# Kernel optimization log

Measured on AMD Instinct MI355X. Metric: run time of the kernel, lower is better.

## Reference

```python
import jax, jax.numpy as jnp
import numpy as np
from jax import lax

B, P, N, D, L, H = 16, 8192, 1024, 384, 12, 6
HD = D // H
K_NEI = 5          # HomogeneityLoss k
KL_RATIO = 1.0


def setup_inputs() -> dict:
    key = jax.random.key(0)
    ks = jax.random.split(key, 10)
    s = lambda i, shape, sc=0.02: (jax.random.normal(ks[i], shape, jnp.float32) * sc)
    return dict(
        pts=jax.random.normal(ks[0], (B, P, 3), jnp.float32),
        grid=jax.random.normal(ks[1], (B, N, 3), jnp.float32),
        embed_w=s(2, (3, D), 0.1),
        proj_w=s(3, (D, 3), 0.1),
        ln1_w=jnp.ones((L, D)), ln1_b=jnp.zeros((L, D)),
        qkv_w=s(4, (L, D, 3 * D)), qkv_b=jnp.zeros((L, 3 * D)),
        attn_w=s(5, (L, D, D)), attn_b=jnp.zeros((L, D)),
        ln2_w=jnp.ones((L, D)), ln2_b=jnp.zeros((L, D)),
        mlp_w1=s(6, (L, D, 4 * D)), mlp_b1=jnp.zeros((L, 4 * D)),
        mlp_w2=s(7, (L, 4 * D, D)), mlp_b2=jnp.zeros((L, D)),
    )


def _ln(x, w, b):
    m = jnp.mean(x, -1, keepdims=True)
    v = jnp.var(x, -1, keepdims=True)
    return (x - m) * lax.rsqrt(v + 1e-5) * w + b


def _transformer(x, params):
    def layer(x, p):
        l1w, l1b, qw, qb, aw, ab, l2w, l2b, m1w, m1b, m2w, m2b = p
        h = _ln(x, l1w, l1b)
        qkv = h @ qw + qb                                   # [B,N,3D]
        q, k, v = jnp.split(qkv, 3, axis=-1)
        rs = lambda t: t.reshape(B, N, H, HD).transpose(0, 2, 1, 3)  # [B,H,N,HD]
        q, k, v = rs(q), rs(k), rs(v)
        att = jax.nn.softmax(jnp.einsum('bhnd,bhmd->bhnm', q, k) / np.sqrt(HD), axis=-1)
        o = jnp.einsum('bhnm,bhmd->bhnd', att, v).transpose(0, 2, 1, 3).reshape(B, N, D)
        x = x + (o @ aw + ab)
        h = _ln(x, l2w, l2b)
        x = x + (jax.nn.gelu(h @ m1w + m1b) @ m2w + m2b)
        return x, None
    x, _ = lax.scan(layer, x, params)
    return x


def _fps(points):  # points: [P,3] -> N int32 indices (farthest point sampling)
    def body(carry, _):
        dists, last = carry
        d = jnp.sum((points - points[last]) ** 2, axis=-1)
        dists = jnp.minimum(dists, d)
        return (dists, jnp.argmax(dists).astype(jnp.int32)), last
    init = (jnp.full((points.shape[0],), 1e10, points.dtype), jnp.int32(0))
    (_, _), idxs = lax.scan(body, init, None, length=N)
    return idxs


def reference(pts, grid, embed_w, proj_w, ln1_w, ln1_b, qkv_w, qkv_b,
              attn_w, attn_b, ln2_w, ln2_b, mlp_w1, mlp_b1, mlp_w2, mlp_b2):
    params = (ln1_w, ln1_b, qkv_w, qkv_b, attn_w, attn_b,
              ln2_w, ln2_b, mlp_w1, mlp_b1, mlp_w2, mlp_b2)
    x = grid @ embed_w                                      # [B,N,D]
    x = _transformer(x, params)
    pred = x @ proj_w                                       # [B,N,3]

    # FPS centers from the raw point cloud
    idxs = jax.vmap(_fps)(pts)                              # [B,N]
    centers = jnp.take_along_axis(pts, idxs[..., None], axis=1)  # [B,N,3]

    # Chamfer L1 (symmetric mean of nearest-neighbor L2 norms)
    d = jnp.linalg.norm(pred[:, :, None, :] - centers[:, None, :, :], axis=-1)  # [B,N,N]
    rec = 0.5 * (d.min(axis=2).mean(axis=1) + d.min(axis=1).mean(axis=1))       # [B]

    # Homogeneity: mean dist of K_NEI nearest neighbors -> softmax -> KL(q||p)
    dd = jnp.linalg.norm(pred[:, :, None, :] - pred[:, None, :, :], axis=-1)    # [B,N,N]
    neg_vals, _ = lax.top_k(-dd, K_NEI + 1)                 # smallest K+1 dists
    mean_d = (-neg_vals[..., 1:]).mean(axis=-1)             # drop self -> [B,N]
    logp = jax.nn.log_softmax(mean_d, axis=-1)
    q = 1.0 / N
    kl = jnp.sum(q * (jnp.log(q) - logp), axis=-1)          # [B]

    return rec.mean(), KL_RATIO * kl.mean()
```

## Files before the change

kernel.cpp:

```cpp
#include <hip/hip_runtime.h>
#include <math.h>

#define B_   16
#define P_   8192
#define N_   1024
#define D_   384
#define L_   12
#define H_   6
#define HD_  64
#define M_   (B_*N_)
#define DQKV_ (3*D_)
#define DH_   (4*D_)

typedef unsigned short ushort_t;
typedef unsigned long long u64_t;
typedef __attribute__((ext_vector_type(8))) short short8;
typedef __attribute__((ext_vector_type(4))) float floatx4;

__device__ __forceinline__ ushort_t f2bf(float f) {
    unsigned u = __float_as_uint(f);
    unsigned rounding = 0x7fffu + ((u >> 16) & 1u);
    return (ushort_t)((u + rounding) >> 16);
}
__device__ __forceinline__ float bf2f(ushort_t u) {
    return __uint_as_float(((unsigned)u) << 16);
}

__global__ __launch_bounds__(D_) void embed_kernel(const float* __restrict__ g,
                                                   const float* __restrict__ ew,
                                                   float* __restrict__ X) {
    int m = blockIdx.x;
    int d = threadIdx.x;
    float g0 = g[m*3+0], g1 = g[m*3+1], g2 = g[m*3+2];
    X[(size_t)m*D_ + d] = g0*ew[0*D_+d] + g1*ew[1*D_+d] + g2*ew[2*D_+d];
}

__global__ __launch_bounds__(256) void transcast_kernel(const float* __restrict__ W,
                                                        ushort_t* __restrict__ Wt,
                                                        int K, int Nc) {
    __shared__ float t[32][33];
    const float* Wl = W + (size_t)blockIdx.z*K*Nc;
    ushort_t* Wtl = Wt + (size_t)blockIdx.z*K*Nc;
    int n0 = blockIdx.x*32, k0 = blockIdx.y*32;
    int tx = threadIdx.x & 31, ty = threadIdx.x >> 5;
#pragma unroll
    for (int j = 0; j < 32; j += 8)
        t[ty+j][tx] = Wl[(size_t)(k0+ty+j)*Nc + n0+tx];
    __syncthreads();
#pragma unroll
    for (int j = 0; j < 32; j += 8)
        Wtl[(size_t)(n0+ty+j)*K + k0+tx] = f2bf(t[tx][ty+j]);
}

__global__ __launch_bounds__(256) void ln_kernel(const float* __restrict__ Xin,
                                                 const float* __restrict__ w,
                                                 const float* __restrict__ bvec,
                                                 ushort_t* __restrict__ out) {
    int wid = threadIdx.x >> 6, lane = threadIdx.x & 63;
    int row = blockIdx.x*4 + wid;
    const float* xr = Xin + (size_t)row*D_;
    float v[6];
#pragma unroll
    for (int i = 0; i < 6; i++) v[i] = xr[lane + i*64];
    float s = 0.f;
#pragma unroll
    for (int i = 0; i < 6; i++) s += v[i];
#pragma unroll
    for (int off = 32; off; off >>= 1) s += __shfl_xor(s, off, 64);
    float mean = s * (1.0f/(float)D_);
    float vs = 0.f;
#pragma unroll
    for (int i = 0; i < 6; i++) { float d = v[i]-mean; vs += d*d; }
#pragma unroll
    for (int off = 32; off; off >>= 1) vs += __shfl_xor(vs, off, 64);
    float var = vs * (1.0f/(float)D_);
    float rstd = 1.0f / sqrtf(var + 1e-5f);
    ushort_t* orow = out + (size_t)row*D_;
#pragma unroll
    for (int i = 0; i < 6; i++) {
        int e = lane + i*64;
        orow[e] = f2bf((v[i]-mean)*rstd*w[e] + bvec[e]);
    }
}

__device__ __forceinline__ float gelu_f(float x) {
    const float c = 0.7978845608028654f;
    float x3 = x*x*x;
    return 0.5f*x*(1.0f + tanhf(c*(x + 0.044715f*x3)));
}

template<int EPI>
__global__ __launch_bounds__(256) void mfma_gemm(const ushort_t* __restrict__ A,
                                                 const ushort_t* __restrict__ Wt,
                                                 const float* __restrict__ bias,
                                                 void* __restrict__ Cout,
                                                 ushort_t* __restrict__ VT,
                                                 int K, int Nc) {
    __shared__ __attribute__((aligned(16))) ushort_t smem[2*128*32];
    ushort_t* smA = smem;
    ushort_t* smB = smem + 128*32;
    int tid = threadIdx.x;
    int lane = tid & 63, w = tid >> 6;
    int wm = w >> 1, wn = w & 1;
    int L = lane & 15, G = lane >> 4;
    int rowBase = blockIdx.y * 128, colBase = blockIdx.x * 128;

    floatx4 acc[4][4];
#pragma unroll
    for (int i = 0; i < 4; i++)
#pragma unroll
        for (int j = 0; j < 4; j++) acc[i][j] = (floatx4){0.f,0.f,0.f,0.f};

    int sr = tid >> 2;
    int kc = tid & 3;
    const ushort_t* Ag = A  + (size_t)(rowBase + sr)*K + kc*8;
    const ushort_t* Bg = Wt + (size_t)(colBase + sr)*K + kc*8;
    size_t step64 = (size_t)64*K;

    short8 ra0, ra1, rb0, rb1;
    ra0 = *(const short8*)(Ag);
    ra1 = *(const short8*)(Ag + step64);
    rb0 = *(const short8*)(Bg);
    rb1 = *(const short8*)(Bg + step64);

    for (int k0 = 0; k0 < K; k0 += 32) {
        __syncthreads();
        *(short8*)(smA + sr*32 + kc*8)        = ra0;
        *(short8*)(smA + (64+sr)*32 + kc*8)   = ra1;
        *(short8*)(smB + sr*32 + kc*8)        = rb0;
        *(short8*)(smB + (64+sr)*32 + kc*8)   = rb1;
        __syncthreads();
        if (k0 + 32 < K) {
            ra0 = *(const short8*)(Ag + k0 + 32);
            ra1 = *(const short8*)(Ag + step64 + k0 + 32);
            rb0 = *(const short8*)(Bg + k0 + 32);
            rb1 = *(const short8*)(Bg + step64 + k0 + 32);
        }
        short8 af[4], bfr[4];
#pragma unroll
        for (int t = 0; t < 4; t++) {
            af[t]  = *(const short8*)(smA + (wm*64 + t*16 + L)*32 + G*8);
            bfr[t] = *(const short8*)(smB + (wn*64 + t*16 + L)*32 + G*8);
        }
#pragma unroll
        for (int mt = 0; mt < 4; mt++)
#pragma unroll
            for (int nt = 0; nt < 4; nt++)
                acc[mt][nt] = __builtin_amdgcn_mfma_f32_16x16x32_bf16(
                    af[mt], bfr[nt], acc[mt][nt], 0, 0, 0);
        __syncthreads();
    }

    __syncthreads();

    if (EPI == 3 && colBase >= 2*D_) {
        int cBase = colBase + wn*64 + L;
        int rBase = rowBase + wm*64 + G*4;
#pragma unroll
        for (int nt = 0; nt < 4; nt++) {
            int col = cBase + nt*16;
            float bv = bias[col];
            int hh = (col - 2*D_) >> 6, d = (col - 2*D_) & 63;
#pragma unroll
            for (int mt = 0; mt < 4; mt++) {
#pragma unroll
                for (int r = 0; r < 4; r++) {
                    int row = rBase + mt*16 + r;
                    int b = row >> 10, n = row & 1023;
                    VT[(((size_t)b*H_ + hh)*64 + d)*N_ + n] = f2bf(acc[mt][nt][r] + bv);
                }
            }
        }
    } else if (EPI == 1) {
        float* fs = (float*)smem + w*1024;
        int orow = lane >> 2, c4 = lane & 3;
#pragma unroll
        for (int mt = 0; mt < 4; mt++) {
#pragma unroll
            for (int nt = 0; nt < 4; nt++) {
                float bv = bias[colBase + wn*64 + nt*16 + L];
#pragma unroll
                for (int r = 0; r < 4; r++)
                    fs[(G*4+r)*64 + nt*16 + L] = acc[mt][nt][r] + bv;
            }
            float* og = (float*)Cout + (size_t)(rowBase + wm*64 + mt*16 + orow)*Nc
                        + colBase + wn*64;
#pragma unroll
            for (int kk = 0; kk < 4; kk++) {
                float4 sv = *(float4*)(fs + orow*64 + kk*16 + c4*4);
                float4 gv = *(float4*)(og + kk*16 + c4*4);
                gv.x += sv.x; gv.y += sv.y; gv.z += sv.z; gv.w += sv.w;
                *(float4*)(og + kk*16 + c4*4) = gv;
            }
        }
    } else {
        ushort_t* us = smem + w*1152;
        int orow = lane >> 2, oc = lane & 3;
#pragma unroll
        for (int mt = 0; mt < 4; mt++) {
#pragma unroll
            for (int nt = 0; nt < 4; nt++) {
                float bv = bias[colBase + wn*64 + nt*16 + L];
#pragma unroll
                for (int r = 0; r < 4; r++) {
                    float v = acc[mt][nt][r] + bv;
                    if (EPI == 2) v = gelu_f(v);
                    us[(G*4+r)*72 + nt*16 + L] = f2bf(v);
                }
            }
            short8 o0 = *(short8*)(us + orow*72 + oc*8);
            short8 o1 = *(short8*)(us + orow*72 + 32 + oc*8);
            ushort_t* og = (ushort_t*)Cout + (size_t)(rowBase + wm*64 + mt*16 + orow)*Nc
                           + colBase + wn*64;
            *(short8*)(og + oc*8) = o0;
            *(short8*)(og + 32 + oc*8) = o1;
        }
    }
}

#define LPAD 72
__global__ __launch_bounds__(256) void fattn_kernel(const ushort_t* __restrict__ QKV,
                                                    const ushort_t* __restrict__ VT,
                                                    ushort_t* __restrict__ O) {
    __shared__ __attribute__((aligned(16))) ushort_t Ks[64*LPAD];
    __shared__ __attribute__((aligned(16))) ushort_t Vs[64*LPAD];
    __shared__ __attribute__((aligned(16))) ushort_t Pw[4*16*LPAD];
    int b = blockIdx.z, h = blockIdx.y;
    int qBase = blockIdx.x * 64;
    int tid = threadIdx.x;
    int lane = tid & 63, w = tid >> 6;
    int L = lane & 15, G = lane >> 4;

    short8 qf[2];
    {
        const ushort_t* qp = QKV + ((size_t)(b*N_ + qBase + w*16 + L))*DQKV_ + h*HD_ + G*8;
        qf[0] = *(const short8*)(qp);
        qf[1] = *(const short8*)(qp + 32);
    }

    floatx4 oacc[4];
#pragma unroll
    for (int nt = 0; nt < 4; nt++) oacc[nt] = (floatx4){0.f,0.f,0.f,0.f};
    float mrow[4], lrow[4];
#pragma unroll
    for (int r = 0; r < 4; r++) { mrow[r] = -3.0e38f; lrow[r] = 0.f; }

    ushort_t* pw = Pw + w*16*LPAD;
    const ushort_t* Kbase = QKV + (size_t)b*N_*DQKV_ + D_ + h*HD_;
    const ushort_t* Vbase = VT + ((size_t)b*H_ + h)*64*N_;

    int srow = tid >> 3;
    int dc   = tid & 7;
    const ushort_t* Kg0 = Kbase + (size_t)srow*DQKV_ + dc*8;
    const ushort_t* Kg1 = Kbase + (size_t)(srow+32)*DQKV_ + dc*8;
    const ushort_t* Vg0 = Vbase + (size_t)srow*N_ + dc*8;
    const ushort_t* Vg1 = Vbase + (size_t)(srow+32)*N_ + dc*8;

    short8 rk0, rk1, rv0, rv1;
    rk0 = *(const short8*)(Kg0);
    rk1 = *(const short8*)(Kg1);
    rv0 = *(const short8*)(Vg0);
    rv1 = *(const short8*)(Vg1);

    for (int kt = 0; kt < N_/64; kt++) {
        __syncthreads();
        *(short8*)(Ks + srow*LPAD + dc*8)       = rk0;
        *(short8*)(Ks + (srow+32)*LPAD + dc*8)  = rk1;
        *(short8*)(Vs + srow*LPAD + dc*8)       = rv0;
        *(short8*)(Vs + (srow+32)*LPAD + dc*8)  = rv1;
        __syncthreads();
        if (kt + 1 < N_/64) {
            rk0 = *(const short8*)(Kg0 + (size_t)(kt+1)*64*DQKV_);
            rk1 = *(const short8*)(Kg1 + (size_t)(kt+1)*64*DQKV_);
            rv0 = *(const short8*)(Vg0 + (kt+1)*64);
            rv1 = *(const short8*)(Vg1 + (kt+1)*64);
        }

        floatx4 sc[4];
#pragma unroll
        for (int ct = 0; ct < 4; ct++) sc[ct] = (floatx4){0.f,0.f,0.f,0.f};
#pragma unroll
        for (int ks = 0; ks < 2; ks++)
#pragma unroll
            for (int ct = 0; ct < 4; ct++) {
                short8 bf = *(const short8*)(Ks + (ct*16 + L)*LPAD + ks*32 + G*8);
                sc[ct] = __builtin_amdgcn_mfma_f32_16x16x32_bf16(qf[ks], bf, sc[ct], 0, 0, 0);
            }

        float rmax[4], rsum[4];
#pragma unroll
        for (int r = 0; r < 4; r++) {
#pragma unroll
            for (int ct = 0; ct < 4; ct++) sc[ct][r] *= 0.125f;
            rmax[r] = fmaxf(fmaxf(sc[0][r], sc[1][r]), fmaxf(sc[2][r], sc[3][r]));
        }
#pragma unroll
        for (int off = 1; off < 16; off <<= 1)
#pragma unroll
            for (int r = 0; r < 4; r++) rmax[r] = fmaxf(rmax[r], __shfl_xor(rmax[r], off, 64));
        float corr[4];
#pragma unroll
        for (int r = 0; r < 4; r++) {
            float mn = fmaxf(mrow[r], rmax[r]);
            corr[r] = __expf(mrow[r] - mn);
            mrow[r] = mn;
            rsum[r] = 0.f;
#pragma unroll
            for (int ct = 0; ct < 4; ct++) {
                float p = __expf(sc[ct][r] - mn);
                sc[ct][r] = p;
                rsum[r] += p;
            }
        }
#pragma unroll
        for (int off = 1; off < 16; off <<= 1)
#pragma unroll
            for (int r = 0; r < 4; r++) rsum[r] += __shfl_xor(rsum[r], off, 64);
#pragma unroll
        for (int r = 0; r < 4; r++) lrow[r] = lrow[r]*corr[r] + rsum[r];

#pragma unroll
        for (int ct = 0; ct < 4; ct++)
#pragma unroll
            for (int r = 0; r < 4; r++)
                pw[(G*4 + r)*LPAD + ct*16 + L] = f2bf(sc[ct][r]);
#pragma unroll
        for (int nt = 0; nt < 4; nt++)
#pragma unroll
            for (int r = 0; r < 4; r++) oacc[nt][r] *= corr[r];

#pragma unroll
        for (int ks = 0; ks < 2; ks++) {
            short8 pf = *(const short8*)(pw + L*LPAD + ks*32 + G*8);
#pragma unroll
            for (int nt = 0; nt < 4; nt++) {
                short8 vf = *(const short8*)(Vs + (nt*16 + L)*LPAD + ks*32 + G*8);
                oacc[nt] = __builtin_amdgcn_mfma_f32_16x16x32_bf16(pf, vf, oacc[nt], 0, 0, 0);
            }
        }
    }

    float inv[4];
#pragma unroll
    for (int r = 0; r < 4; r++) inv[r] = 1.0f / lrow[r];
#pragma unroll
    for (int nt = 0; nt < 4; nt++)
#pragma unroll
        for (int r = 0; r < 4; r++)
            pw[(G*4 + r)*LPAD + nt*16 + L] = f2bf(oacc[nt][r]*inv[r]);
    int orow = lane >> 2, oc = lane & 3;
    short8 o0 = *(short8*)(pw + orow*LPAD + oc*8);
    short8 o1 = *(short8*)(pw + orow*LPAD + 32 + oc*8);
    ushort_t* og = O + (size_t)(b*N_ + qBase + w*16 + orow)*D_ + h*HD_;
    *(short8*)(og + oc*8) = o0;
    *(short8*)(og + 32 + oc*8) = o1;
}

__global__ __launch_bounds__(256) void proj_kernel(const float* __restrict__ X,
                                                   const float* __restrict__ pw,
                                                   float* __restrict__ pred) {
    int wid = threadIdx.x >> 6, lane = threadIdx.x & 63;
    int m = blockIdx.x*4 + wid;
    const float* xr = X + (size_t)m*D_;
    float a0 = 0.f, a1 = 0.f, a2 = 0.f;
#pragma unroll
    for (int i = 0; i < 6; i++) {
        int k = lane + i*64;
        float xv = xr[k];
        a0 += xv*pw[k*3+0]; a1 += xv*pw[k*3+1]; a2 += xv*pw[k*3+2];
    }
#pragma unroll
    for (int off = 32; off; off >>= 1) {
        a0 += __shfl_xor(a0, off, 64);
        a1 += __shfl_xor(a1, off, 64);
        a2 += __shfl_xor(a2, off, 64);
    }
    if (lane == 0) {
        pred[m*3+0] = a0; pred[m*3+1] = a1; pred[m*3+2] = a2;
    }
}

__global__ __launch_bounds__(512) void fps_kernel(const float* __restrict__ pts,
                                                  float* __restrict__ centers) {
    __shared__ float Lx[P_], Ly[P_], Lz[P_];
    __shared__ u64_t slot[2][8];
    int b = blockIdx.x, t = threadIdx.x;
    const float* pb = pts + (size_t)b*P_*3;
    float px[16], py[16], pz[16], dist[16];
#pragma unroll
    for (int j = 0; j < 16; j++) {
        int p = j*512 + t;
        px[j] = pb[p*3+0]; py[j] = pb[p*3+1]; pz[j] = pb[p*3+2];
        Lx[p] = px[j]; Ly[p] = py[j]; Lz[p] = pz[j];
        dist[j] = 1e10f;
    }
    int wid = t >> 6, lane = t & 63;
    int winner = 0;
    __syncthreads();
    for (int it = 0; it < N_; it++) {
        float lx = Lx[winner], ly = Ly[winner], lz = Lz[winner];
        if (t == 0) {
            float* c = centers + ((size_t)b*N_ + it)*3;
            c[0] = lx; c[1] = ly; c[2] = lz;
        }
        float bd = -1.0f; int bj = 0;
#pragma unroll
        for (int j = 0; j < 16; j++) {
            float dx = __fsub_rn(px[j], lx);
            float dy = __fsub_rn(py[j], ly);
            float dz = __fsub_rn(pz[j], lz);
            float d = __fadd_rn(__fadd_rn(__fmul_rn(dx,dx), __fmul_rn(dy,dy)), __fmul_rn(dz,dz));
            d = fminf(dist[j], d);
            dist[j] = d;
            bool gt = d > bd;
            bd = gt ? d : bd;
            bj = gt ? j : bj;
        }
        u64_t best = ((u64_t)__float_as_uint(bd) << 32)
                   | (unsigned)(~(unsigned)(bj*512 + t));
#pragma unroll
        for (int off = 32; off; off >>= 1) {
            u64_t o = __shfl_xor(best, off, 64);
            best = (o > best) ? o : best;
        }
        int par = it & 1;
        if (lane == 0) slot[par][wid] = best;
        __syncthreads();
        u64_t v = slot[par][lane & 7];
#pragma unroll
        for (int off = 1; off < 8; off <<= 1) {
            u64_t o = __shfl_xor(v, off, 64);
            v = (o > v) ? o : v;
        }
        winner = (int)(~(unsigned)(v & 0xFFFFFFFFull));
    }
}

__global__ __launch_bounds__(256) void nnmin_kernel(const float* __restrict__ Asrc,
                                                    const float* __restrict__ Bsrc,
                                                    float* __restrict__ outmin) {
    int b = blockIdx.y;
    int i = blockIdx.x*256 + threadIdx.x;
    __shared__ float tile[256][3];
    const float* ar = Asrc + ((size_t)b*N_ + i)*3;
    float ax = ar[0], ay = ar[1], az = ar[2];
    float best = 3.0e38f;
    for (int j0 = 0; j0 < N_; j0 += 256) {
        __syncthreads();
        const float* br = Bsrc + ((size_t)b*N_ + j0 + threadIdx.x)*3;
        tile[threadIdx.x][0] = br[0]; tile[threadIdx.x][1] = br[1]; tile[threadIdx.x][2] = br[2];
        __syncthreads();
        for (int j = 0; j < 256; j++) {
            float dx = ax - tile[j][0], dy = ay - tile[j][1], dz = az - tile[j][2];
            float d = dx*dx + dy*dy + dz*dz;
            best = fminf(best, d);
        }
    }
    outmin[(size_t)b*N_ + i] = sqrtf(best);
}

__global__ __launch_bounds__(256) void knn_kernel(const float* __restrict__ Pp,
                                                  float* __restrict__ mean_d) {
    int b = blockIdx.y;
    int i = blockIdx.x*256 + threadIdx.x;
    __shared__ float tile[256][3];
    const float* ar = Pp + ((size_t)b*N_ + i)*3;
    float ax = ar[0], ay = ar[1], az = ar[2];
    float s[6];
#pragma unroll
    for (int q = 0; q < 6; q++) s[q] = 3.0e38f;
    for (int j0 = 0; j0 < N_; j0 += 256) {
        __syncthreads();
        const float* br = Pp + ((size_t)b*N_ + j0 + threadIdx.x)*3;
        tile[threadIdx.x][0] = br[0]; tile[threadIdx.x][1] = br[1]; tile[threadIdx.x][2] = br[2];
        __syncthreads();
        for (int j = 0; j < 256; j++) {
            float dx = ax - tile[j][0], dy = ay - tile[j][1], dz = az - tile[j][2];
            float d = dx*dx + dy*dy + dz*dz;
            if (d < s[5]) {
                s[5] = d;
#pragma unroll
                for (int q = 5; q > 0; q--)
                    if (s[q] < s[q-1]) { float tmp = s[q]; s[q] = s[q-1]; s[q-1] = tmp; }
            }
        }
    }
    float msum = sqrtf(s[1]) + sqrtf(s[2]) + sqrtf(s[3]) + sqrtf(s[4]) + sqrtf(s[5]);
    mean_d[(size_t)b*N_ + i] = msum * 0.2f;
}

__global__ __launch_bounds__(256) void kl_kernel(const float* __restrict__ md,
                                                 float* __restrict__ klb) {
    int b = blockIdx.x, t = threadIdx.x;
    const float* row = md + (size_t)b*N_;
    float v[4];
#pragma unroll
    for (int i = 0; i < 4; i++) v[i] = row[t + i*256];
    float mx = fmaxf(fmaxf(v[0], v[1]), fmaxf(v[2], v[3]));
#pragma unroll
    for (int off = 32; off; off >>= 1) mx = fmaxf(mx, __shfl_xor(mx, off, 64));
    __shared__ float redm[4], rse[4], rsx[4];
    int wid = t >> 6, lane = t & 63;
    if (lane == 0) redm[wid] = mx;
    __syncthreads();
    mx = fmaxf(fmaxf(redm[0], redm[1]), fmaxf(redm[2], redm[3]));
    float se = 0.f, sx = 0.f;
#pragma unroll
    for (int i = 0; i < 4; i++) { se += expf(v[i]-mx); sx += v[i]; }
#pragma unroll
    for (int off = 32; off; off >>= 1) { se += __shfl_xor(se, off, 64); sx += __shfl_xor(sx, off, 64); }
    if (lane == 0) { rse[wid] = se; rsx[wid] = sx; }
    __syncthreads();
    if (t == 0) {
        float SE = rse[0]+rse[1]+rse[2]+rse[3];
        float SX = rsx[0]+rsx[1]+rsx[2]+rsx[3];
        klb[b] = mx + logf(SE) - SX*(1.0f/(float)N_) - logf((float)N_);
    }
}

__global__ __launch_bounds__(256) void final_kernel(const float* __restrict__ rma,
                                                    const float* __restrict__ rmb,
                                                    const float* __restrict__ klb,
                                                    float* __restrict__ out) {
    int t = threadIdx.x;
    float s = 0.f;
    for (int i = t; i < B_*N_; i += 256) s += rma[i] + rmb[i];
#pragma unroll
    for (int off = 32; off; off >>= 1) s += __shfl_xor(s, off, 64);
    __shared__ float red[4];
    int wid = t >> 6, lane = t & 63;
    if (lane == 0) red[wid] = s;
    __syncthreads();
    if (t == 0) {
        float S = red[0]+red[1]+red[2]+red[3];
        out[0] = 0.5f*S/(float)(B_*N_);
        float K = 0.f;
        for (int b = 0; b < B_; b++) K += klb[b];
        out[1] = K/(float)B_;
    }
}

extern "C" void kernel_launch(void* const* d_in, const int* in_sizes, int n_in,
                              void* d_out, int out_size, void* d_ws, size_t ws_size,
                              hipStream_t stream) {
    (void)in_sizes; (void)n_in; (void)out_size; (void)ws_size;
    const float* pts     = (const float*)d_in[0];
    const float* grid    = (const float*)d_in[1];
    const float* embed_w = (const float*)d_in[2];
    const float* proj_w  = (const float*)d_in[3];
    const float* ln1_w   = (const float*)d_in[4];
    const float* ln1_b   = (const float*)d_in[5];
    const float* qkv_w   = (const float*)d_in[6];
    const float* qkv_b   = (const float*)d_in[7];
    const float* attn_w  = (const float*)d_in[8];
    const float* attn_b  = (const float*)d_in[9];
    const float* ln2_w   = (const float*)d_in[10];
    const float* ln2_b   = (const float*)d_in[11];
    const float* mlp_w1  = (const float*)d_in[12];
    const float* mlp_b1  = (const float*)d_in[13];
    const float* mlp_w2  = (const float*)d_in[14];
    const float* mlp_b2  = (const float*)d_in[15];
    float* out = (float*)d_out;

    float*    X     = (float*)d_ws;
    ushort_t* Hb16  = (ushort_t*)(X + (size_t)M_*D_);
    ushort_t* BIG16 = Hb16 + (size_t)M_*D_;
    ushort_t* VT    = BIG16 + (size_t)M_*DH_;
    ushort_t* WQ    = VT  + (size_t)B_*H_*HD_*N_;
    ushort_t* WA    = WQ  + (size_t)L_*DQKV_*D_;
    ushort_t* WM1   = WA  + (size_t)L_*D_*D_;
    ushort_t* WM2   = WM1 + (size_t)L_*DH_*D_;
    float*    PRED  = (float*)(WM2 + (size_t)L_*D_*DH_);
    float*    CENT  = PRED + (size_t)M_*3;
    float*    RMA   = CENT + (size_t)B_*N_*3;
    float*    RMB   = RMA  + (size_t)B_*N_;
    float*    MEAND = RMB  + (size_t)B_*N_;
    float*    KLB   = MEAND + (size_t)B_*N_;

    transcast_kernel<<<dim3(DQKV_/32, D_/32,  L_), 256, 0, stream>>>(qkv_w,  WQ,  D_,  DQKV_);
    transcast_kernel<<<dim3(D_/32,    D_/32,  L_), 256, 0, stream>>>(attn_w, WA,  D_,  D_);
    transcast_kernel<<<dim3(DH_/32,   D_/32,  L_), 256, 0, stream>>>(mlp_w1, WM1, D_,  DH_);
    transcast_kernel<<<dim3(D_/32,    DH_/32, L_), 256, 0, stream>>>(mlp_w2, WM2, DH_, D_);

    fps_kernel<<<B_, 512, 0, stream>>>(pts, CENT);

    embed_kernel<<<M_, D_, 0, stream>>>(grid, embed_w, X);

    for (int l = 0; l < L_; l++) {
        ln_kernel<<<M_/4, 256, 0, stream>>>(X, ln1_w + l*D_, ln1_b + l*D_, Hb16);
        mfma_gemm<3><<<dim3(DQKV_/128, M_/128), 256, 0, stream>>>(
            Hb16, WQ + (size_t)l*DQKV_*D_, qkv_b + l*DQKV_, BIG16, VT, D_, DQKV_);
        fattn_kernel<<<dim3(N_/64, H_, B_), 256, 0, stream>>>(BIG16, VT, Hb16);
        mfma_gemm<1><<<dim3(D_/128, M_/128), 256, 0, stream>>>(
            Hb16, WA + (size_t)l*D_*D_, attn_b + l*D_, X, nullptr, D_, D_);
        ln_kernel<<<M_/4, 256, 0, stream>>>(X, ln2_w + l*D_, ln2_b + l*D_, Hb16);
        mfma_gemm<2><<<dim3(DH_/128, M_/128), 256, 0, stream>>>(
            Hb16, WM1 + (size_t)l*DH_*D_, mlp_b1 + l*DH_, BIG16, nullptr, D_, DH_);
        mfma_gemm<1><<<dim3(D_/128, M_/128), 256, 0, stream>>>(
            BIG16, WM2 + (size_t)l*D_*DH_, mlp_b2 + l*D_, X, nullptr, DH_, D_);
    }

    proj_kernel<<<M_/4, 256, 0, stream>>>(X, proj_w, PRED);

    nnmin_kernel<<<dim3(N_/256, B_), 256, 0, stream>>>(PRED, CENT, RMA);
    nnmin_kernel<<<dim3(N_/256, B_), 256, 0, stream>>>(CENT, PRED, RMB);
    knn_kernel<<<dim3(N_/256, B_), 256, 0, stream>>>(PRED, MEAND);
    kl_kernel<<<B_, 256, 0, stream>>>(MEAND, KLB);
    final_kernel<<<1, 256, 0, stream>>>(RMA, RMB, KLB, out);
}
```

Baseline: 4.619 ms.

## Split FPS into chunks piggybacked on transformer GEMM and attention launches

Removes the standalone serial FPS kernel and runs it in 29-iteration chunks inside extra blocks appended to the QKV GEMM, attention and MLP1 GEMM grids. Per-batch distance state and the current winner persist in global memory between chunks. The goal is to hide the long single-block-per-batch FPS latency behind the transformer work. In exchange, each chunk reloads point coordinates from global memory every iteration instead of holding them in LDS or registers. The extra blocks, placed at the end of the grid, may also lengthen the tail of each kernel they join.

```diff
diff --git a/kernel.cpp b/kernel.cpp
--- a/kernel.cpp
+++ b/kernel.cpp
@@ -11,6 +11,7 @@
 #define M_   (B_*N_)
 #define DQKV_ (3*D_)
 #define DH_   (4*D_)
+#define FPS_IT 29
 
 typedef unsigned short ushort_t;
 typedef unsigned long long u64_t;
@@ -24,6 +25,71 @@
 }
 __device__ __forceinline__ float bf2f(ushort_t u) {
     return __uint_as_float(((unsigned)u) << 16);
+}
+
+__device__ __forceinline__ void fps_chunk(const float* __restrict__ pts,
+                                          float* __restrict__ FDIST,
+                                          int* __restrict__ FWIN,
+                                          float* __restrict__ CENT,
+                                          int b, int start, u64_t* slot) {
+    int t = threadIdx.x;
+    int wid = t >> 6, lane = t & 63;
+    const float* pb = pts + (size_t)b*P_*3;
+    float* fd = FDIST + (size_t)b*P_;
+    float dist[32];
+    int winner;
+    if (start == 0) {
+#pragma unroll
+        for (int j = 0; j < 32; j++) dist[j] = 1e10f;
+        winner = 0;
+    } else {
+#pragma unroll
+        for (int j = 0; j < 32; j++) dist[j] = fd[j*256 + t];
+        winner = FWIN[b];
+    }
+    int end = start + FPS_IT; if (end > N_) end = N_;
+    for (int it = start; it < end; it++) {
+        const float* wc = pb + winner*3;
+        float lx = wc[0], ly = wc[1], lz = wc[2];
+        if (t == 0) {
+            float* c = CENT + ((size_t)b*N_ + it)*3;
+            c[0] = lx; c[1] = ly; c[2] = lz;
+        }
+        float bd = -1.0f; int bj = 0;
+#pragma unroll
+        for (int j = 0; j < 32; j++) {
+            int p = j*256 + t;
+            float dx = __fsub_rn(pb[p*3+0], lx);
+            float dy = __fsub_rn(pb[p*3+1], ly);
+            float dz = __fsub_rn(pb[p*3+2], lz);
+            float d = __fadd_rn(__fadd_rn(__fmul_rn(dx,dx), __fmul_rn(dy,dy)), __fmul_rn(dz,dz));
+            d = fminf(dist[j], d);
+            dist[j] = d;
+            bool gt = d > bd;
+            bd = gt ? d : bd;
+            bj = gt ? j : bj;
+        }
+        u64_t best = ((u64_t)__float_as_uint(bd) << 32)
+                   | (unsigned)(~(unsigned)(bj*256 + t));
+#pragma unroll
+        for (int off = 32; off; off >>= 1) {
+            u64_t o = __shfl_xor(best, off, 64);
+            best = (o > best) ? o : best;
+        }
+        int par = it & 1;
+        if (lane == 0) slot[par*4 + wid] = best;
+        __syncthreads();
+        u64_t v = slot[par*4 + (lane & 3)];
+#pragma unroll
+        for (int off = 1; off < 4; off <<= 1) {
+            u64_t o = __shfl_xor(v, off, 64);
+            v = (o > v) ? o : v;
+        }
+        winner = (int)(~(unsigned)(v & 0xFFFFFFFFull));
+    }
+#pragma unroll
+    for (int j = 0; j < 32; j++) fd[j*256 + t] = dist[j];
+    if (t == 0) FWIN[b] = winner;
 }
 
 __global__ __launch_bounds__(D_) void embed_kernel(const float* __restrict__ g,
@@ -95,8 +161,22 @@
                                                  const float* __restrict__ bias,
                                                  void* __restrict__ Cout,
                                                  ushort_t* __restrict__ VT,
+                                                 const float* __restrict__ pts,
+                                                 float* __restrict__ FDIST,
+                                                 int* __restrict__ FWIN,
+                                                 float* __restrict__ CENT,
+                                                 int fps_start,
                                                  int K, int Nc) {
     __shared__ __attribute__((aligned(16))) ushort_t smem[2*128*32];
+    int ncols = Nc >> 7;
+    if ((int)blockIdx.x >= ncols) {
+        if ((int)blockIdx.y == 0) {
+            int b = (int)blockIdx.x - ncols;
+            if (b < B_ && fps_start >= 0 && fps_start < N_)
+                fps_chunk(pts, FDIST, FWIN, CENT, b, fps_start, (u64_t*)smem);
+        }
+        return;
+    }
     ushort_t* smA = smem;
     ushort_t* smB = smem + 128*32;
     int tid = threadIdx.x;
@@ -221,10 +301,23 @@
 #define LPAD 72
 __global__ __launch_bounds__(256) void fattn_kernel(const ushort_t* __restrict__ QKV,
                                                     const ushort_t* __restrict__ VT,
-                                                    ushort_t* __restrict__ O) {
+                                                    ushort_t* __restrict__ O,
+                                                    const float* __restrict__ pts,
+                                                    float* __restrict__ FDIST,
+                                                    int* __restrict__ FWIN,
+                                                    float* __restrict__ CENT,
+                                                    int fps_start) {
     __shared__ __attribute__((aligned(16))) ushort_t Ks[64*LPAD];
     __shared__ __attribute__((aligned(16))) ushort_t Vs[64*LPAD];
     __shared__ __attribute__((aligned(16))) ushort_t Pw[4*16*LPAD];
+    if ((int)blockIdx.x >= N_/64) {
+        if (blockIdx.y == 0 && blockIdx.z == 0) {
+            int b = (int)blockIdx.x - N_/64;
+            if (b < B_ && fps_start >= 0 && fps_start < N_)
+                fps_chunk(pts, FDIST, FWIN, CENT, b, fps_start, (u64_t*)Ks);
+        }
+        return;
+    }
     int b = blockIdx.z, h = blockIdx.y;
     int qBase = blockIdx.x * 64;
     int tid = threadIdx.x;
@@ -377,62 +470,6 @@
     }
     if (lane == 0) {
         pred[m*3+0] = a0; pred[m*3+1] = a1; pred[m*3+2] = a2;
-    }
-}
-
-__global__ __launch_bounds__(512) void fps_kernel(const float* __restrict__ pts,
-                                                  float* __restrict__ centers) {
-    __shared__ float Lx[P_], Ly[P_], Lz[P_];
-    __shared__ u64_t slot[2][8];
-    int b = blockIdx.x, t = threadIdx.x;
-    const float* pb = pts + (size_t)b*P_*3;
-    float px[16], py[16], pz[16], dist[16];
-#pragma unroll
-    for (int j = 0; j < 16; j++) {
-        int p = j*512 + t;
-        px[j] = pb[p*3+0]; py[j] = pb[p*3+1]; pz[j] = pb[p*3+2];
-        Lx[p] = px[j]; Ly[p] = py[j]; Lz[p] = pz[j];
-        dist[j] = 1e10f;
-    }
-    int wid = t >> 6, lane = t & 63;
-    int winner = 0;
-    __syncthreads();
-    for (int it = 0; it < N_; it++) {
-        float lx = Lx[winner], ly = Ly[winner], lz = Lz[winner];
-        if (t == 0) {
-            float* c = centers + ((size_t)b*N_ + it)*3;
-            c[0] = lx; c[1] = ly; c[2] = lz;
-        }
-        float bd = -1.0f; int bj = 0;
-#pragma unroll
-        for (int j = 0; j < 16; j++) {
-            float dx = __fsub_rn(px[j], lx);
-            float dy = __fsub_rn(py[j], ly);
-            float dz = __fsub_rn(pz[j], lz);
-            float d = __fadd_rn(__fadd_rn(__fmul_rn(dx,dx), __fmul_rn(dy,dy)), __fmul_rn(dz,dz));
-            d = fminf(dist[j], d);
-            dist[j] = d;
-            bool gt = d > bd;
-            bd = gt ? d : bd;
-            bj = gt ? j : bj;
-        }
-        u64_t best = ((u64_t)__float_as_uint(bd) << 32)
-                   | (unsigned)(~(unsigned)(bj*512 + t));
-#pragma unroll
-        for (int off = 32; off; off >>= 1) {
-            u64_t o = __shfl_xor(best, off, 64);
-            best = (o > best) ? o : best;
-        }
-        int par = it & 1;
-        if (lane == 0) slot[par][wid] = best;
-        __syncthreads();
-        u64_t v = slot[par][lane & 7];
-#pragma unroll
-        for (int off = 1; off < 8; off <<= 1) {
-            u64_t o = __shfl_xor(v, off, 64);
-            v = (o > v) ? o : v;
-        }
-        winner = (int)(~(unsigned)(v & 0xFFFFFFFFull));
     }
 }
 
@@ -576,28 +613,34 @@
     float*    RMB   = RMA  + (size_t)B_*N_;
     float*    MEAND = RMB  + (size_t)B_*N_;
     float*    KLB   = MEAND + (size_t)B_*N_;
+    float*    FDIST = KLB + B_;
+    int*      FWIN  = (int*)(FDIST + (size_t)B_*P_);
 
     transcast_kernel<<<dim3(DQKV_/32, D_/32,  L_), 256, 0, stream>>>(qkv_w,  WQ,  D_,  DQKV_);
     transcast_kernel<<<dim3(D_/32,    D_/32,  L_), 256, 0, stream>>>(attn_w, WA,  D_,  D_);
     transcast_kernel<<<dim3(DH_/32,   D_/32,  L_), 256, 0, stream>>>(mlp_w1, WM1, D_,  DH_);
     transcast_kernel<<<dim3(D_/32,    DH_/32, L_), 256, 0, stream>>>(mlp_w2, WM2, DH_, D_);
 
-    fps_kernel<<<B_, 512, 0, stream>>>(pts, CENT);
-
     embed_kernel<<<M_, D_, 0, stream>>>(grid, embed_w, X);
 
+    int fc = 0;
     for (int l = 0; l < L_; l++) {
         ln_kernel<<<M_/4, 256, 0, stream>>>(X, ln1_w + l*D_, ln1_b + l*D_, Hb16);
-        mfma_gemm<3><<<dim3(DQKV_/128, M_/128), 256, 0, stream>>>(
-            Hb16, WQ + (size_t)l*DQKV_*D_, qkv_b + l*DQKV_, BIG16, VT, D_, DQKV_);
-        fattn_kernel<<<dim3(N_/64, H_, B_), 256, 0, stream>>>(BIG16, VT, Hb16);
+        mfma_gemm<3><<<dim3(DQKV_/128 + B_, M_/128), 256, 0, stream>>>(
+            Hb16, WQ + (size_t)l*DQKV_*D_, qkv_b + l*DQKV_, BIG16, VT,
+            pts, FDIST, FWIN, CENT, (fc++)*FPS_IT, D_, DQKV_);
+        fattn_kernel<<<dim3(N_/64 + B_, H_, B_), 256, 0, stream>>>(
+            BIG16, VT, Hb16, pts, FDIST, FWIN, CENT, (fc++)*FPS_IT);
         mfma_gemm<1><<<dim3(D_/128, M_/128), 256, 0, stream>>>(
-            Hb16, WA + (size_t)l*D_*D_, attn_b + l*D_, X, nullptr, D_, D_);
+            Hb16, WA + (size_t)l*D_*D_, attn_b + l*D_, X, nullptr,
+            pts, FDIST, FWIN, CENT, -1, D_, D_);
         ln_kernel<<<M_/4, 256, 0, stream>>>(X, ln2_w + l*D_, ln2_b + l*D_, Hb16);
-        mfma_gemm<2><<<dim3(DH_/128, M_/128), 256, 0, stream>>>(
-            Hb16, WM1 + (size_t)l*DH_*D_, mlp_b1 + l*DH_, BIG16, nullptr, D_, DH_);
+        mfma_gemm<2><<<dim3(DH_/128 + B_, M_/128), 256, 0, stream>>>(
+            Hb16, WM1 + (size_t)l*DH_*D_, mlp_b1 + l*DH_, BIG16, nullptr,
+            pts, FDIST, FWIN, CENT, (fc++)*FPS_IT, D_, DH_);
         mfma_gemm<1><<<dim3(D_/128, M_/128), 256, 0, stream>>>(
-            BIG16, WM2 + (size_t)l*D_*DH_, mlp_b2 + l*D_, X, nullptr, DH_, D_);
+            BIG16, WM2 + (size_t)l*D_*DH_, mlp_b2 + l*D_, X, nullptr,
+            pts, FDIST, FWIN, CENT, -1, DH_, D_);
     }
 
     proj_kernel<<<M_/4, 256, 0, stream>>>(X, proj_w, PRED);
```

Result: slower. 6.529 ms (+41.4%).
